# Optimization experiments

Hardware: AMD Instinct MI355X
Metric: run time of the kernel (lower is better)

The kernel has to match this reference:

```python
import jax, jax.numpy as jnp
import numpy as np


def setup_inputs() -> dict:
    key = jax.random.key(0)
    k1, k2, k3 = jax.random.split(key, 3)
    B, F, K = 16384, 512, 1000
    D = jax.random.normal(k1, (B, F), dtype=jnp.float32)
    weight = jax.random.normal(k2, (K, F), dtype=jnp.float32)  # (out_features, in_features)
    gamma = jax.random.uniform(k3, (K,), dtype=jnp.float32)
    return {"D": D, "weight": weight, "gamma": gamma}


def reference(D, weight, gamma):
    # Squared Euclidean distance from each row of D to each centroid (row of weight),
    # computed via ||a||^2 + ||b||^2 - 2 a.b (mathematically equal to the broadcast
    # subtract-square-sum in the original torch forward with d_view=None).
    d_sq = jnp.sum(D * D, axis=1, keepdims=True)            # (B, 1)
    w_sq = jnp.sum(weight * weight, axis=1)                  # (K,)
    cross = jnp.einsum('bf,kf->bk', D, weight)               # (B, K)
    dist_sq = d_sq + w_sq[None, :] - 2.0 * cross             # (B, K)
    return -dist_sq * gamma                                  # (B, K)
```

## Files before the change

kernel.cpp:

```cpp
#include <hip/hip_runtime.h>
#include <hip/hip_bf16.h>
#include <stdint.h>

#define B_ROWS 16384
#define F_DIM  512
#define K_OUT  1000
#define K_PAD  1024

#define BM 128
#define BN 128
#define BK 64

typedef __attribute__((ext_vector_type(4))) float f32x4;
typedef __attribute__((ext_vector_type(8))) short short8;
typedef unsigned short u16;
typedef unsigned int   u32;

#define OFF_DB   0
#define OFF_WB   16777216
#define OFF_DSQ  (16777216 + 1048576)
#define OFF_WSQ  (16777216 + 1048576 + 65536)

__device__ __forceinline__ u16 f2bf(float f) {
  union { float f; u32 u; } v; v.f = f;
  u32 u = v.u;
  u32 r = (u + 0x7fffu + ((u >> 16) & 1u)) >> 16;
  return (u16)r;
}

__global__ void prep_D(const float* __restrict__ D, u16* __restrict__ Db,
                       float* __restrict__ dsq) {
  int w    = threadIdx.x >> 6;
  int lane = threadIdx.x & 63;
  int row  = blockIdx.x * 4 + w;
  const float* src = D + (size_t)row * F_DIM + lane * 8;
  float4 v0 = *(const float4*)src;
  float4 v1 = *(const float4*)(src + 4);
  float s = v0.x*v0.x + v0.y*v0.y + v0.z*v0.z + v0.w*v0.w
          + v1.x*v1.x + v1.y*v1.y + v1.z*v1.z + v1.w*v1.w;
#pragma unroll
  for (int off = 32; off >= 1; off >>= 1) s += __shfl_xor(s, off);
  if (lane == 0) dsq[row] = s;
  uint4 p;
  p.x = (u32)f2bf(v0.x) | ((u32)f2bf(v0.y) << 16);
  p.y = (u32)f2bf(v0.z) | ((u32)f2bf(v0.w) << 16);
  p.z = (u32)f2bf(v1.x) | ((u32)f2bf(v1.y) << 16);
  p.w = (u32)f2bf(v1.z) | ((u32)f2bf(v1.w) << 16);
  *(uint4*)(Db + (size_t)row * F_DIM + lane * 8) = p;
}

__global__ void prep_W(const float* __restrict__ W, u16* __restrict__ Wb,
                       float* __restrict__ wsq) {
  int w    = threadIdx.x >> 6;
  int lane = threadIdx.x & 63;
  int row  = blockIdx.x * 4 + w;
  uint4 p; p.x = p.y = p.z = p.w = 0u;
  float s = 0.f;
  if (row < K_OUT) {
    const float* src = W + (size_t)row * F_DIM + lane * 8;
    float4 v0 = *(const float4*)src;
    float4 v1 = *(const float4*)(src + 4);
    s = v0.x*v0.x + v0.y*v0.y + v0.z*v0.z + v0.w*v0.w
      + v1.x*v1.x + v1.y*v1.y + v1.z*v1.z + v1.w*v1.w;
    p.x = (u32)f2bf(v0.x) | ((u32)f2bf(v0.y) << 16);
    p.y = (u32)f2bf(v0.z) | ((u32)f2bf(v0.w) << 16);
    p.z = (u32)f2bf(v1.x) | ((u32)f2bf(v1.y) << 16);
    p.w = (u32)f2bf(v1.z) | ((u32)f2bf(v1.w) << 16);
  }
#pragma unroll
  for (int off = 32; off >= 1; off >>= 1) s += __shfl_xor(s, off);
  if (lane == 0) wsq[row] = s;
  *(uint4*)(Wb + (size_t)row * F_DIM + lane * 8) = p;
}

__device__ __forceinline__ void gload_lds16(const void* g, void* l) {
  __builtin_amdgcn_global_load_lds(
      (const __attribute__((address_space(1))) void*)g,
      (__attribute__((address_space(3))) void*)l,
      16, 0, 0);
}

__global__ __launch_bounds__(256) void gemm_eps(
    const u16* __restrict__ A,
    const u16* __restrict__ Bw,
    const float* __restrict__ dsq,
    const float* __restrict__ wsq,
    const float* __restrict__ gamma,
    float* __restrict__ out) {
  __shared__ u16 sA[BM * BK];
  __shared__ u16 sB[BN * BK];
  char* sAc = (char*)sA;
  char* sBc = (char*)sB;

  int tid  = threadIdx.x;
  int w    = tid >> 6;
  int lane = tid & 63;
  int lr   = lane & 15;
  int lk   = lane >> 4;
  int wm   = w >> 1;
  int wn   = w & 1;

  int bid = blockIdx.x;
  int cpx = gridDim.x >> 3;
  int wg  = (bid & 7) * cpx + (bid >> 3);
  int mt  = wg >> 3;
  int nt  = wg & 7;
  int m0  = mt * BM;
  int n0  = nt * BN;

  const u16* Ag = A  + (size_t)m0 * F_DIM;
  const u16* Bg = Bw + (size_t)n0 * F_DIM;

  f32x4 acc[4][4];
#pragma unroll
  for (int i = 0; i < 4; ++i)
#pragma unroll
    for (int j = 0; j < 4; ++j)
      acc[i][j] = (f32x4){0.f, 0.f, 0.f, 0.f};

  int rs  = w * 8 + (lane >> 3);
  int s8  = lane & 7;

  for (int kt = 0; kt < F_DIM / BK; ++kt) {
    int kbase = kt * BK;
#pragma unroll
    for (int i = 0; i < 4; ++i) {
      int r  = i * 32 + rs;
      int sc = s8 ^ (r & 7);
      gload_lds16(Ag + (size_t)r * F_DIM + kbase + sc * 8, sAc + i * 4096 + w * 1024);
      gload_lds16(Bg + (size_t)r * F_DIM + kbase + sc * 8, sBc + i * 4096 + w * 1024);
    }
    __syncthreads();
#pragma unroll
    for (int t = 0; t < 2; ++t) {
      short8 af[4], bfr[4];
#pragma unroll
      for (int mi = 0; mi < 4; ++mi) {
        int r = wm * 64 + mi * 16 + lr;
        int s = (t * 4 + lk) ^ (r & 7);
        af[mi] = *(const short8*)(sAc + r * 128 + (s << 4));
      }
#pragma unroll
      for (int ni = 0; ni < 4; ++ni) {
        int r = wn * 64 + ni * 16 + lr;
        int s = (t * 4 + lk) ^ (r & 7);
        bfr[ni] = *(const short8*)(sBc + r * 128 + (s << 4));
      }
#pragma unroll
      for (int mi = 0; mi < 4; ++mi)
#pragma unroll
        for (int ni = 0; ni < 4; ++ni)
          acc[mi][ni] = __builtin_amdgcn_mfma_f32_16x16x32_bf16(
              af[mi], bfr[ni], acc[mi][ni], 0, 0, 0);
    }
    __syncthreads();
  }

  float dl[4][4];
#pragma unroll
  for (int mi = 0; mi < 4; ++mi) {
    int r0 = m0 + wm * 64 + mi * 16 + lk * 4;
#pragma unroll
    for (int j = 0; j < 4; ++j) dl[mi][j] = dsq[r0 + j];
  }
#pragma unroll
  for (int ni = 0; ni < 4; ++ni) {
    int col = n0 + wn * 64 + ni * 16 + lr;
    if (col < K_OUT) {
      float g  = gamma[col];
      float wq = wsq[col];
#pragma unroll
      for (int mi = 0; mi < 4; ++mi) {
        int r0 = m0 + wm * 64 + mi * 16 + lk * 4;
#pragma unroll
        for (int j = 0; j < 4; ++j) {
          out[(size_t)(r0 + j) * K_OUT + col] =
              g * (2.0f * acc[mi][ni][j] - dl[mi][j] - wq);
        }
      }
    }
  }
}

extern "C" void kernel_launch(void* const* d_in, const int* in_sizes, int n_in,
                              void* d_out, int out_size, void* d_ws, size_t ws_size,
                              hipStream_t stream) {
  const float* D     = (const float*)d_in[0];
  const float* W     = (const float*)d_in[1];
  const float* gamma = (const float*)d_in[2];
  float* out = (float*)d_out;
  char*  ws  = (char*)d_ws;

  u16*   Db  = (u16*)(ws + OFF_DB);
  u16*   Wb  = (u16*)(ws + OFF_WB);
  float* dsq = (float*)(ws + OFF_DSQ);
  float* wsq = (float*)(ws + OFF_WSQ);

  prep_D<<<B_ROWS / 4, 256, 0, stream>>>(D, Db, dsq);
  prep_W<<<K_PAD / 4, 256, 0, stream>>>(W, Wb, wsq);

  gemm_eps<<<(B_ROWS / BM) * (K_PAD / BN), 256, 0, stream>>>(
      Db, Wb, dsq, wsq, gamma, out);
}
```

Baseline: 47.48 us.

## Use 256x256 tiles with double-buffered LDS pipeline and staged coalesced epilogue

Enlarges the GEMM tile to 256x256 with 512 threads (8 waves) and double-buffers the LDS so each K-step's global-to-LDS loads are issued in quarters between MFMA groups, with barriers and setprio controlling the interleave. The epilogue now writes results through LDS in 64-row chunks so the output goes out as row-contiguous float4 stores instead of scattered scalars. The goals are more data reuse per tile, load/compute overlap, and coalesced output writes. In exchange it uses 128KB of LDS and 128 accumulator registers per thread, which limits occupancy to one block per CU. The grid shrinks to 256 blocks, which may underfill the GPU's CUs.

```diff
diff --git a/kernel.cpp b/kernel.cpp
--- a/kernel.cpp
+++ b/kernel.cpp
@@ -7,8 +7,8 @@
 #define K_OUT  1000
 #define K_PAD  1024
 
-#define BM 128
-#define BN 128
+#define BM 256
+#define BN 256
 #define BK 64
 
 typedef __attribute__((ext_vector_type(4))) float f32x4;
@@ -80,103 +80,146 @@
       16, 0, 0);
 }
 
-__global__ __launch_bounds__(256) void gemm_eps(
+
+#define READ_A(QM)                                                             \
+  _Pragma("unroll") for (int mi2 = 0; mi2 < 4; ++mi2)                          \
+  _Pragma("unroll") for (int kk = 0; kk < 2; ++kk) {                           \
+    int r = wm * 128 + ((QM) * 4 + mi2) * 16 + lr;                             \
+    a[mi2][kk] = *(const short8*)(sAc + r * 128 +                              \
+                                  ((((kk << 2) + lk4) ^ (r & 7)) << 4));       \
+  }
+
+#define READ_B(QN)                                                             \
+  _Pragma("unroll") for (int ni2 = 0; ni2 < 2; ++ni2)                          \
+  _Pragma("unroll") for (int kk = 0; kk < 2; ++kk) {                           \
+    int r = wn * 64 + ((QN) * 2 + ni2) * 16 + lr;                              \
+    b[ni2][kk] = *(const short8*)(sBc + r * 128 +                              \
+                                  ((((kk << 2) + lk4) ^ (r & 7)) << 4));       \
+  }
+
+#define STAGE(Q)                                                               \
+  if (t < 7) {                                                                 \
+    int r  = (Q) * 64 + srow;                                                  \
+    int sc = s8 ^ (r & 7);                                                     \
+    gload_lds16(Ag + (size_t)r * F_DIM + kbn + sc * 8,                         \
+                sAn + (Q) * 8192 + w * 1024);                                  \
+    gload_lds16(Bg + (size_t)r * F_DIM + kbn + sc * 8,                         \
+                sBn + (Q) * 8192 + w * 1024);                                  \
+  }
+
+#define MFMA16(QM, QN)                                                         \
+  __builtin_amdgcn_s_barrier();                                                \
+  asm volatile("s_waitcnt lgkmcnt(0)" ::: "memory");                           \
+  __builtin_amdgcn_sched_barrier(0);                                           \
+  __builtin_amdgcn_s_setprio(1);                                               \
+  _Pragma("unroll") for (int mi2 = 0; mi2 < 4; ++mi2)                          \
+  _Pragma("unroll") for (int ni2 = 0; ni2 < 2; ++ni2)                          \
+  _Pragma("unroll") for (int kk = 0; kk < 2; ++kk)                             \
+    acc[(QM)*4 + mi2][(QN)*2 + ni2] =                                          \
+        __builtin_amdgcn_mfma_f32_16x16x32_bf16(                               \
+            a[mi2][kk], b[ni2][kk], acc[(QM)*4 + mi2][(QN)*2 + ni2], 0, 0, 0); \
+  __builtin_amdgcn_s_setprio(0);                                               \
+  __builtin_amdgcn_s_barrier();
+
+__global__ __launch_bounds__(512, 2) void gemm_eps(
     const u16* __restrict__ A,
     const u16* __restrict__ Bw,
     const float* __restrict__ dsq,
     const float* __restrict__ wsq,
     const float* __restrict__ gamma,
     float* __restrict__ out) {
-  __shared__ u16 sA[BM * BK];
-  __shared__ u16 sB[BN * BK];
-  char* sAc = (char*)sA;
-  char* sBc = (char*)sB;
-
-  int tid  = threadIdx.x;
-  int w    = tid >> 6;
-  int lane = tid & 63;
-  int lr   = lane & 15;
-  int lk   = lane >> 4;
-  int wm   = w >> 1;
-  int wn   = w & 1;
-
-  int bid = blockIdx.x;
-  int cpx = gridDim.x >> 3;
-  int wg  = (bid & 7) * cpx + (bid >> 3);
-  int mt  = wg >> 3;
-  int nt  = wg & 7;
-  int m0  = mt * BM;
-  int n0  = nt * BN;
+  __shared__ __align__(16) char lds[131072];
+
+  const int tid  = threadIdx.x;
+  const int w    = tid >> 6;
+  const int lane = tid & 63;
+  const int lr   = lane & 15;
+  const int lk4  = lane >> 4;
+  const int wm   = w >> 2;
+  const int wn   = w & 3;
+
+  const int bid = blockIdx.x;
+  const int wg  = (bid & 7) * 32 + (bid >> 3);
+  const int mt  = wg >> 2;
+  const int nt  = wg & 3;
+  const int m0  = mt * BM;
+  const int n0  = nt * BN;
 
   const u16* Ag = A  + (size_t)m0 * F_DIM;
   const u16* Bg = Bw + (size_t)n0 * F_DIM;
 
-  f32x4 acc[4][4];
-#pragma unroll
-  for (int i = 0; i < 4; ++i)
-#pragma unroll
-    for (int j = 0; j < 4; ++j)
-      acc[i][j] = (f32x4){0.f, 0.f, 0.f, 0.f};
-
-  int rs  = w * 8 + (lane >> 3);
-  int s8  = lane & 7;
-
-  for (int kt = 0; kt < F_DIM / BK; ++kt) {
-    int kbase = kt * BK;
-#pragma unroll
-    for (int i = 0; i < 4; ++i) {
-      int r  = i * 32 + rs;
-      int sc = s8 ^ (r & 7);
-      gload_lds16(Ag + (size_t)r * F_DIM + kbase + sc * 8, sAc + i * 4096 + w * 1024);
-      gload_lds16(Bg + (size_t)r * F_DIM + kbase + sc * 8, sBc + i * 4096 + w * 1024);
+  const int srow = w * 8 + (lane >> 3);
+  const int s8   = lane & 7;
+
+  f32x4 acc[8][4];
+#pragma unroll
+  for (int i = 0; i < 8; ++i)
+#pragma unroll
+    for (int j = 0; j < 4; ++j) acc[i][j] = (f32x4){0.f, 0.f, 0.f, 0.f};
+
+#pragma unroll
+  for (int q = 0; q < 4; ++q) {
+    int r  = q * 64 + srow;
+    int sc = s8 ^ (r & 7);
+    gload_lds16(Ag + (size_t)r * F_DIM + sc * 8, lds + q * 8192 + w * 1024);
+    gload_lds16(Bg + (size_t)r * F_DIM + sc * 8, lds + 32768 + q * 8192 + w * 1024);
+  }
+  __syncthreads();
+
+#pragma unroll 2
+  for (int t = 0; t < 8; ++t) {
+    char* sAc = lds + (t & 1) * 65536;
+    char* sBc = sAc + 32768;
+    char* sAn = lds + ((t + 1) & 1) * 65536;
+    char* sBn = sAn + 32768;
+    const int kbn = (t + 1) * 64;
+    short8 a[4][2], b[2][2];
+
+    READ_A(0) READ_B(0) STAGE(0) MFMA16(0, 0)
+    READ_B(1)           STAGE(1) MFMA16(0, 1)
+    READ_A(1)           STAGE(2) MFMA16(1, 1)
+    READ_B(0)           STAGE(3) MFMA16(1, 0)
+
+    __syncthreads();
+  }
+
+  float g_[4], wq_[4];
+#pragma unroll
+  for (int ni = 0; ni < 4; ++ni) {
+    int col = n0 + wn * 64 + ni * 16 + lr;
+    g_[ni]  = (col < K_OUT) ? gamma[col] : 0.f;
+    wq_[ni] = (col < K_OUT) ? wsq[col]   : 0.f;
+  }
+  float* ch = (float*)lds;
+  const int rl = tid >> 3;
+  const int cb = (tid & 7) << 2;
+#pragma unroll
+  for (int c = 0; c < 4; ++c) {
+    __syncthreads();
+    if (wm == (c >> 1)) {
+#pragma unroll
+      for (int mi2 = 0; mi2 < 4; ++mi2) {
+        const int mi    = ((c & 1) << 2) + mi2;
+        const int row_l = mi2 * 16 + lk4 * 4;
+        const int grow  = m0 + c * 64 + row_l;
+#pragma unroll
+        for (int j = 0; j < 4; ++j) {
+          float dq = dsq[grow + j];
+#pragma unroll
+          for (int ni = 0; ni < 4; ++ni) {
+            ch[(row_l + j) * 260 + wn * 64 + ni * 16 + lr] =
+                g_[ni] * (2.f * acc[mi][ni][j] - dq - wq_[ni]);
+          }
+        }
+      }
     }
     __syncthreads();
 #pragma unroll
-    for (int t = 0; t < 2; ++t) {
-      short8 af[4], bfr[4];
-#pragma unroll
-      for (int mi = 0; mi < 4; ++mi) {
-        int r = wm * 64 + mi * 16 + lr;
-        int s = (t * 4 + lk) ^ (r & 7);
-        af[mi] = *(const short8*)(sAc + r * 128 + (s << 4));
-      }
-#pragma unroll
-      for (int ni = 0; ni < 4; ++ni) {
-        int r = wn * 64 + ni * 16 + lr;
-        int s = (t * 4 + lk) ^ (r & 7);
-        bfr[ni] = *(const short8*)(sBc + r * 128 + (s << 4));
-      }
-#pragma unroll
-      for (int mi = 0; mi < 4; ++mi)
-#pragma unroll
-        for (int ni = 0; ni < 4; ++ni)
-          acc[mi][ni] = __builtin_amdgcn_mfma_f32_16x16x32_bf16(
-              af[mi], bfr[ni], acc[mi][ni], 0, 0, 0);
-    }
-    __syncthreads();
-  }
-
-  float dl[4][4];
-#pragma unroll
-  for (int mi = 0; mi < 4; ++mi) {
-    int r0 = m0 + wm * 64 + mi * 16 + lk * 4;
-#pragma unroll
-    for (int j = 0; j < 4; ++j) dl[mi][j] = dsq[r0 + j];
-  }
-#pragma unroll
-  for (int ni = 0; ni < 4; ++ni) {
-    int col = n0 + wn * 64 + ni * 16 + lr;
-    if (col < K_OUT) {
-      float g  = gamma[col];
-      float wq = wsq[col];
-#pragma unroll
-      for (int mi = 0; mi < 4; ++mi) {
-        int r0 = m0 + wm * 64 + mi * 16 + lk * 4;
-#pragma unroll
-        for (int j = 0; j < 4; ++j) {
-          out[(size_t)(r0 + j) * K_OUT + col] =
-              g * (2.0f * acc[mi][ni][j] - dl[mi][j] - wq);
-        }
+    for (int s = 0; s < 8; ++s) {
+      int col = cb + s * 32;
+      if (n0 + col < K_OUT) {
+        float4 v = *(const float4*)&ch[rl * 260 + col];
+        *(float4*)&out[(size_t)(m0 + c * 64 + rl) * K_OUT + n0 + col] = v;
       }
     }
   }
@@ -199,6 +242,6 @@
   prep_D<<<B_ROWS / 4, 256, 0, stream>>>(D, Db, dsq);
   prep_W<<<K_PAD / 4, 256, 0, stream>>>(W, Wb, wsq);
 
-  gemm_eps<<<(B_ROWS / BM) * (K_PAD / BN), 256, 0, stream>>>(
+  gemm_eps<<<(B_ROWS / BM) * (K_PAD / BN), 512, 0, stream>>>(
       Db, Wb, dsq, wsq, gamma, out);
 }
```

Result: faster. 44.01 us (-7.3%).
